# Optimization experiments

Hardware: AMD Instinct MI355X
Metric: run time of the kernel (lower is better)

Reference implementation:

```python
import jax, jax.numpy as jnp
import numpy as np


def setup_inputs() -> dict:
    key = jax.random.key(0)
    ks = jax.random.split(key, 7)
    B, C, H, W = 16, 256, 64, 64
    s = 1.0 / np.sqrt(C)  # ~kaiming-uniform scale for 1x1 conv
    return {
        "a": jax.random.normal(ks[0], (B, C, H, W), jnp.float32),
        "wq": jax.random.normal(ks[1], (C, C), jnp.float32) * s,
        "bq": jax.random.normal(ks[2], (C,), jnp.float32) * s,
        "wk": jax.random.normal(ks[3], (C, C), jnp.float32) * s,
        "bk": jax.random.normal(ks[4], (C,), jnp.float32) * s,
        "wv": jax.random.normal(ks[5], (C, C), jnp.float32) * s,
        "bv": jax.random.normal(ks[6], (C,), jnp.float32) * s,
    }


def reference(a, wq, bq, wk, bk, wv, bv):
    # 1x1 conv == per-pixel linear: [B,C,H,W] x [O,C] -> [B,H,W,O]
    def proj(w, b):
        return jnp.einsum('bchw,oc->bhwo', a, w) + b

    q = proj(wq, bq)  # [B,H,W,C]
    k = proj(wk, bk)
    v = proj(wv, bv)

    # unnormalized dot-product attention over the W axis, per row H
    attn = jnp.einsum('bhwc,bhxc->bhwx', q, k)       # [B,H,W,W]
    att_out = jnp.einsum('bhwx,bhxc->bhwc', attn, v)  # [B,H,W,C]

    # permute back to NCHW and residual add
    return a + jnp.transpose(att_out, (0, 3, 1, 2))
```

## Files before the change

kernel.cpp:

```cpp
#include <hip/hip_runtime.h>
#include <hip/hip_bf16.h>

#define NB 16
#define NC 256
#define NH 64
#define NW 64

typedef __attribute__((ext_vector_type(8))) short bf16x8;
typedef __attribute__((ext_vector_type(4))) float f32x4;

__device__ __forceinline__ unsigned short f2bf(float f) {
    union { float f; unsigned int u; } v; v.f = f;
    unsigned int u = v.u;
    u += 0x7fffu + ((u >> 16) & 1u);
    return (unsigned short)(u >> 16);
}

__device__ __forceinline__ int swzT(int row, int col) {
    return row * 256 + ((((col >> 3) ^ (row & 7) ^ ((row >> 3) & 7)) << 3) | (col & 7));
}
__device__ __forceinline__ int swzS(int row, int col) {
    return row * 64 + ((((col >> 3) ^ (row & 7) ^ ((row >> 3) & 7)) << 3) | (col & 7));
}

__global__ void prep(const float* __restrict__ wq, const float* __restrict__ wk,
                     const float* __restrict__ wv,
                     const float* __restrict__ bq, const float* __restrict__ bk,
                     unsigned short* __restrict__ wsb) {
    int bx = blockIdx.x;
    int t = threadIdx.x;
    if (bx < 64) {
        int i = bx * 256 + t;
        float4 v4 = ((const float4*)wv)[i];
        ushort4 u = { f2bf(v4.x), f2bf(v4.y), f2bf(v4.z), f2bf(v4.w) };
        ((ushort4*)(wsb + 65536))[i] = u;
    } else if (bx < 96) {
        int c1_0 = (bx - 64) * 8;
        float acc[8] = {0.f, 0.f, 0.f, 0.f, 0.f, 0.f, 0.f, 0.f};
        for (int o = 0; o < 256; ++o) {
            float wkv = wk[o * 256 + t];
            #pragma unroll
            for (int i = 0; i < 8; ++i)
                acc[i] += wq[o * 256 + c1_0 + i] * wkv;
        }
        #pragma unroll
        for (int i = 0; i < 8; ++i)
            wsb[(c1_0 + i) * 256 + t] = f2bf(acc[i]);
    } else {
        float u = 0.f, v = 0.f;
        #pragma unroll 4
        for (int o = 0; o < 256; ++o) {
            u += bq[o] * wk[o * 256 + t];
            v += bk[o] * wq[o * 256 + t];
        }
        wsb[131072 + t] = f2bf(u);
        wsb[131328 + t] = f2bf(v);
        if (t == 0) {
            float s = 0.f;
            for (int o = 0; o < 256; ++o) s += bq[o] * bk[o];
            *(float*)(wsb + 131584) = s;
        }
    }
}

__launch_bounds__(512, 4)
__global__ void mha_fused(const float* __restrict__ a,
                          const unsigned short* __restrict__ wsb,
                          const float* __restrict__ bv,
                          float* __restrict__ out) {
    __shared__ __align__(16) unsigned short smem[36864];
    __shared__ __align__(16) float uAvA[128];
    unsigned short* AT  = smem;
    unsigned short* TT  = smem + 16384;
    unsigned short* Vs  = smem + 16384;
    unsigned short* ATT = smem + 32768;

    const unsigned short* Gb  = wsb;
    const unsigned short* Wvb = wsb + 65536;
    const unsigned short* ub  = wsb + 131072;
    const unsigned short* vbv = wsb + 131328;

    const int tid = threadIdx.x;
    const int b = blockIdx.x >> 6;
    const int h = blockIdx.x & 63;
    const float* aB = a + (size_t)b * (NC * NH * NW) + h * NW;

    #pragma unroll
    for (int half = 0; half < 2; ++half) {
        int mt = tid + half * 512;
        int c0 = (mt >> 4) << 2;
        int w0 = (mt & 15) << 2;
        float4 r0 = *(const float4*)(aB + (size_t)(c0 + 0) * 4096 + w0);
        float4 r1 = *(const float4*)(aB + (size_t)(c0 + 1) * 4096 + w0);
        float4 r2 = *(const float4*)(aB + (size_t)(c0 + 2) * 4096 + w0);
        float4 r3 = *(const float4*)(aB + (size_t)(c0 + 3) * 4096 + w0);
        const float* f0 = (const float*)&r0;
        const float* f1 = (const float*)&r1;
        const float* f2 = (const float*)&r2;
        const float* f3 = (const float*)&r3;
        #pragma unroll
        for (int j = 0; j < 4; ++j) {
            ushort4 u = { f2bf(f0[j]), f2bf(f1[j]), f2bf(f2[j]), f2bf(f3[j]) };
            *(ushort4*)(AT + swzT(w0 + j, c0)) = u;
        }
    }
    __syncthreads();

    const int wv_ = tid >> 6;
    const int lane = tid & 63;
    const int l15 = lane & 15;
    const int g = lane >> 4;

    {
        f32x4 acc[2][4];
        #pragma unroll
        for (int mi = 0; mi < 2; ++mi)
            #pragma unroll
            for (int n = 0; n < 4; ++n) acc[mi][n] = { 0.f, 0.f, 0.f, 0.f };

        const bool is_u = (wv_ < 4);
        const int uvrow = (wv_ & 3) * 16 + l15;
        const float sval = *(const float*)(wsb + 131584);
        f32x4 accu;
        #pragma unroll
        for (int r = 0; r < 4; ++r) accu[r] = is_u ? sval : 0.f;
        const unsigned short* uvp = is_u ? ub : vbv;

        const unsigned short* g0p = Gb + (wv_ * 32 + l15) * 256 + g * 8;
        const unsigned short* g1p = Gb + (wv_ * 32 + 16 + l15) * 256 + g * 8;
        bf16x8 gf0 = *(const bf16x8*)(g0p);
        bf16x8 gf1 = *(const bf16x8*)(g1p);
        bf16x8 uvf = *(const bf16x8*)(uvp + g * 8);

        #pragma unroll
        for (int kk = 0; kk < 8; ++kk) {
            bf16x8 cg0 = gf0, cg1 = gf1, cuv = uvf;
            if (kk < 7) {
                gf0 = *(const bf16x8*)(g0p + (kk + 1) * 32);
                gf1 = *(const bf16x8*)(g1p + (kk + 1) * 32);
                uvf = *(const bf16x8*)(uvp + (kk + 1) * 32 + g * 8);
            }
            bf16x8 atf[4];
            #pragma unroll
            for (int n = 0; n < 4; ++n)
                atf[n] = *(const bf16x8*)(AT + swzT(n * 16 + l15, kk * 32 + g * 8));
            bf16x8 uvbf = *(const bf16x8*)(AT + swzT(uvrow, kk * 32 + g * 8));
            #pragma unroll
            for (int n = 0; n < 4; ++n)
                acc[0][n] = __builtin_amdgcn_mfma_f32_16x16x32_bf16(cg0, atf[n], acc[0][n], 0, 0, 0);
            #pragma unroll
            for (int n = 0; n < 4; ++n)
                acc[1][n] = __builtin_amdgcn_mfma_f32_16x16x32_bf16(cg1, atf[n], acc[1][n], 0, 0, 0);
            accu = __builtin_amdgcn_mfma_f32_16x16x32_bf16(cuv, uvbf, accu, 0, 0, 0);
        }
        #pragma unroll
        for (int mi = 0; mi < 2; ++mi) {
            int c1_0 = wv_ * 32 + mi * 16 + g * 4;
            #pragma unroll
            for (int n = 0; n < 4; ++n) {
                ushort4 u = { f2bf(acc[mi][n][0]), f2bf(acc[mi][n][1]),
                              f2bf(acc[mi][n][2]), f2bf(acc[mi][n][3]) };
                *(ushort4*)(TT + swzT(n * 16 + l15, c1_0)) = u;
            }
        }
        if (g == 0)
            uAvA[(is_u ? 0 : 64) + uvrow] = accu[0];
    }
    __syncthreads();

    const int wt3 = wv_ >> 1;
    const int xb3 = (wv_ & 1) * 2;
    {
        f32x4 acc3[2] = { { 0, 0, 0, 0 }, { 0, 0, 0, 0 } };
        #pragma unroll
        for (int kk = 0; kk < 8; ++kk) {
            bf16x8 awf = *(const bf16x8*)(AT + swzT(wt3 * 16 + l15, kk * 32 + g * 8));
            #pragma unroll
            for (int j = 0; j < 2; ++j) {
                bf16x8 txf = *(const bf16x8*)(TT + swzT((xb3 + j) * 16 + l15, kk * 32 + g * 8));
                acc3[j] = __builtin_amdgcn_mfma_f32_16x16x32_bf16(txf, awf, acc3[j], 0, 0, 0);
            }
        }
        const int w = wt3 * 16 + l15;
        const float vAw = uAvA[64 + w];
        #pragma unroll
        for (int j = 0; j < 2; ++j) {
            int x0 = (xb3 + j) * 16 + g * 4;
            float4 uq = *(const float4*)&uAvA[x0];
            const float* uqa = (const float*)&uq;
            ushort4 u = { f2bf(acc3[j][0] + uqa[0] + vAw), f2bf(acc3[j][1] + uqa[1] + vAw),
                          f2bf(acc3[j][2] + uqa[2] + vAw), f2bf(acc3[j][3] + uqa[3] + vAw) };
            *(ushort4*)(ATT + swzS(w, x0)) = u;
        }
    }
    __syncthreads();

    float4 res[2][4];
    #pragma unroll
    for (int mi = 0; mi < 2; ++mi) {
        int c = wv_ * 32 + mi * 16 + l15;
        #pragma unroll
        for (int n = 0; n < 4; ++n)
            res[mi][n] = *(const float4*)(aB + (size_t)c * 4096 + n * 16 + g * 4);
    }
    {
        f32x4 acc[2][4];
        #pragma unroll
        for (int mi = 0; mi < 2; ++mi) {
            float bvl = bv[wv_ * 32 + mi * 16 + l15];
            #pragma unroll
            for (int n = 0; n < 4; ++n) acc[mi][n] = { bvl, bvl, bvl, bvl };
        }
        const unsigned short* w0p = Wvb + (wv_ * 32 + l15) * 256 + g * 8;
        const unsigned short* w1p = Wvb + (wv_ * 32 + 16 + l15) * 256 + g * 8;
        bf16x8 wf0 = *(const bf16x8*)(w0p);
        bf16x8 wf1 = *(const bf16x8*)(w1p);
        #pragma unroll
        for (int kk = 0; kk < 8; ++kk) {
            bf16x8 cw0 = wf0, cw1 = wf1;
            if (kk < 7) {
                wf0 = *(const bf16x8*)(w0p + (kk + 1) * 32);
                wf1 = *(const bf16x8*)(w1p + (kk + 1) * 32);
            }
            bf16x8 atx[4];
            #pragma unroll
            for (int n = 0; n < 4; ++n)
                atx[n] = *(const bf16x8*)(AT + swzT(n * 16 + l15, kk * 32 + g * 8));
            #pragma unroll
            for (int n = 0; n < 4; ++n)
                acc[0][n] = __builtin_amdgcn_mfma_f32_16x16x32_bf16(atx[n], cw0, acc[0][n], 0, 0, 0);
            #pragma unroll
            for (int n = 0; n < 4; ++n)
                acc[1][n] = __builtin_amdgcn_mfma_f32_16x16x32_bf16(atx[n], cw1, acc[1][n], 0, 0, 0);
        }
        #pragma unroll
        for (int mi = 0; mi < 2; ++mi) {
            int c = wv_ * 32 + mi * 16 + l15;
            #pragma unroll
            for (int n = 0; n < 4; ++n) {
                ushort4 u = { f2bf(acc[mi][n][0]), f2bf(acc[mi][n][1]),
                              f2bf(acc[mi][n][2]), f2bf(acc[mi][n][3]) };
                *(ushort4*)(Vs + swzS(c, n * 16 + g * 4)) = u;
            }
        }
    }
    __syncthreads();

    {
        f32x4 acc[2][4];
        #pragma unroll
        for (int mi = 0; mi < 2; ++mi)
            #pragma unroll
            for (int n = 0; n < 4; ++n) acc[mi][n] = { 0.f, 0.f, 0.f, 0.f };
        #pragma unroll
        for (int kk = 0; kk < 2; ++kk) {
            bf16x8 attf[4], vsf[2];
            #pragma unroll
            for (int n = 0; n < 4; ++n)
                attf[n] = *(const bf16x8*)(ATT + swzS(n * 16 + l15, kk * 32 + g * 8));
            #pragma unroll
            for (int mi = 0; mi < 2; ++mi)
                vsf[mi] = *(const bf16x8*)(Vs + swzS(wv_ * 32 + mi * 16 + l15, kk * 32 + g * 8));
            #pragma unroll
            for (int mi = 0; mi < 2; ++mi)
                #pragma unroll
                for (int n = 0; n < 4; ++n)
                    acc[mi][n] = __builtin_amdgcn_mfma_f32_16x16x32_bf16(attf[n], vsf[mi], acc[mi][n], 0, 0, 0);
        }
        float* outB = out + (size_t)b * (NC * NH * NW) + h * NW;
        #pragma unroll
        for (int mi = 0; mi < 2; ++mi) {
            int c = wv_ * 32 + mi * 16 + l15;
            float* po = outB + (size_t)c * 4096;
            #pragma unroll
            for (int n = 0; n < 4; ++n) {
                int w0 = n * 16 + g * 4;
                float4 o4;
                o4.x = res[mi][n].x + acc[mi][n][0];
                o4.y = res[mi][n].y + acc[mi][n][1];
                o4.z = res[mi][n].z + acc[mi][n][2];
                o4.w = res[mi][n].w + acc[mi][n][3];
                *(float4*)(po + w0) = o4;
            }
        }
    }
}

extern "C" void kernel_launch(void* const* d_in, const int* in_sizes, int n_in,
                              void* d_out, int out_size, void* d_ws, size_t ws_size,
                              hipStream_t stream) {
    (void)in_sizes; (void)n_in; (void)out_size; (void)ws_size;
    const float* a  = (const float*)d_in[0];
    const float* wq = (const float*)d_in[1];
    const float* bq = (const float*)d_in[2];
    const float* wk = (const float*)d_in[3];
    const float* bk = (const float*)d_in[4];
    const float* wv = (const float*)d_in[5];
    const float* bv = (const float*)d_in[6];
    float* out = (float*)d_out;
    unsigned short* wsb = (unsigned short*)d_ws;

    prep<<<dim3(97), dim3(256), 0, stream>>>(wq, wk, wv, bq, bk, wsb);
    mha_fused<<<dim3(NB * NH), dim3(512), 0, stream>>>(a, wsb, bv, out);
}
```

Baseline: 94.86 us.

## Fuse V projection into first GEMM loop and widen prep kernel grid

Moves the V projection MFMAs into the same k-loop as the folded Wq^T Wk projection, so the AT fragments are loaded from LDS once and used by both. This removes one pass over AT and lets the V accumulators live across the attention-score stage. The residual loads of `a` are issued earlier, before the score write. The prep kernel now uses one block per output row of the folded weight matrix (321 blocks instead of 97), which spreads the weight setup across more blocks. The cost is 32 more live accumulator registers per thread, which may lower occupancy under launch bounds (512,4) or cause spills.

```diff
diff --git a/kernel.cpp b/kernel.cpp
--- a/kernel.cpp
+++ b/kernel.cpp
@@ -29,24 +29,13 @@
                      unsigned short* __restrict__ wsb) {
     int bx = blockIdx.x;
     int t = threadIdx.x;
-    if (bx < 64) {
-        int i = bx * 256 + t;
-        float4 v4 = ((const float4*)wv)[i];
-        ushort4 u = { f2bf(v4.x), f2bf(v4.y), f2bf(v4.z), f2bf(v4.w) };
-        ((ushort4*)(wsb + 65536))[i] = u;
-    } else if (bx < 96) {
-        int c1_0 = (bx - 64) * 8;
-        float acc[8] = {0.f, 0.f, 0.f, 0.f, 0.f, 0.f, 0.f, 0.f};
-        for (int o = 0; o < 256; ++o) {
-            float wkv = wk[o * 256 + t];
-            #pragma unroll
-            for (int i = 0; i < 8; ++i)
-                acc[i] += wq[o * 256 + c1_0 + i] * wkv;
-        }
-        #pragma unroll
-        for (int i = 0; i < 8; ++i)
-            wsb[(c1_0 + i) * 256 + t] = f2bf(acc[i]);
-    } else {
+    if (bx < 256) {
+        float acc = 0.f;
+        #pragma unroll 8
+        for (int o = 0; o < 256; ++o)
+            acc += wq[o * 256 + bx] * wk[o * 256 + t];
+        wsb[bx * 256 + t] = f2bf(acc);
+    } else if (bx == 256) {
         float u = 0.f, v = 0.f;
         #pragma unroll 4
         for (int o = 0; o < 256; ++o) {
@@ -60,6 +49,11 @@
             for (int o = 0; o < 256; ++o) s += bq[o] * bk[o];
             *(float*)(wsb + 131584) = s;
         }
+    } else {
+        int i = (bx - 257) * 256 + t;
+        float4 v4 = ((const float4*)wv)[i];
+        ushort4 u = { f2bf(v4.x), f2bf(v4.y), f2bf(v4.z), f2bf(v4.w) };
+        ((ushort4*)(wsb + 65536))[i] = u;
     }
 }
 
@@ -111,12 +105,20 @@
     const int l15 = lane & 15;
     const int g = lane >> 4;
 
+    f32x4 acc_v[2][4];
+
     {
-        f32x4 acc[2][4];
+        f32x4 acc_t[2][4];
         #pragma unroll
         for (int mi = 0; mi < 2; ++mi)
             #pragma unroll
-            for (int n = 0; n < 4; ++n) acc[mi][n] = { 0.f, 0.f, 0.f, 0.f };
+            for (int n = 0; n < 4; ++n) acc_t[mi][n] = { 0.f, 0.f, 0.f, 0.f };
+        #pragma unroll
+        for (int mi = 0; mi < 2; ++mi) {
+            float bvl = bv[wv_ * 32 + mi * 16 + l15];
+            #pragma unroll
+            for (int n = 0; n < 4; ++n) acc_v[mi][n] = { bvl, bvl, bvl, bvl };
+        }
 
         const bool is_u = (wv_ < 4);
         const int uvrow = (wv_ & 3) * 16 + l15;
@@ -126,18 +128,24 @@
         for (int r = 0; r < 4; ++r) accu[r] = is_u ? sval : 0.f;
         const unsigned short* uvp = is_u ? ub : vbv;
 
-        const unsigned short* g0p = Gb + (wv_ * 32 + l15) * 256 + g * 8;
-        const unsigned short* g1p = Gb + (wv_ * 32 + 16 + l15) * 256 + g * 8;
+        const unsigned short* g0p = Gb  + (wv_ * 32 + l15) * 256 + g * 8;
+        const unsigned short* g1p = Gb  + (wv_ * 32 + 16 + l15) * 256 + g * 8;
+        const unsigned short* w0p = Wvb + (wv_ * 32 + l15) * 256 + g * 8;
+        const unsigned short* w1p = Wvb + (wv_ * 32 + 16 + l15) * 256 + g * 8;
         bf16x8 gf0 = *(const bf16x8*)(g0p);
         bf16x8 gf1 = *(const bf16x8*)(g1p);
+        bf16x8 wf0 = *(const bf16x8*)(w0p);
+        bf16x8 wf1 = *(const bf16x8*)(w1p);
         bf16x8 uvf = *(const bf16x8*)(uvp + g * 8);
 
         #pragma unroll
         for (int kk = 0; kk < 8; ++kk) {
-            bf16x8 cg0 = gf0, cg1 = gf1, cuv = uvf;
+            bf16x8 cg0 = gf0, cg1 = gf1, cw0 = wf0, cw1 = wf1, cuv = uvf;
             if (kk < 7) {
                 gf0 = *(const bf16x8*)(g0p + (kk + 1) * 32);
                 gf1 = *(const bf16x8*)(g1p + (kk + 1) * 32);
+                wf0 = *(const bf16x8*)(w0p + (kk + 1) * 32);
+                wf1 = *(const bf16x8*)(w1p + (kk + 1) * 32);
                 uvf = *(const bf16x8*)(uvp + (kk + 1) * 32 + g * 8);
             }
             bf16x8 atf[4];
@@ -147,10 +155,16 @@
             bf16x8 uvbf = *(const bf16x8*)(AT + swzT(uvrow, kk * 32 + g * 8));
             #pragma unroll
             for (int n = 0; n < 4; ++n)
-                acc[0][n] = __builtin_amdgcn_mfma_f32_16x16x32_bf16(cg0, atf[n], acc[0][n], 0, 0, 0);
-            #pragma unroll
-            for (int n = 0; n < 4; ++n)
-                acc[1][n] = __builtin_amdgcn_mfma_f32_16x16x32_bf16(cg1, atf[n], acc[1][n], 0, 0, 0);
+                acc_t[0][n] = __builtin_amdgcn_mfma_f32_16x16x32_bf16(cg0, atf[n], acc_t[0][n], 0, 0, 0);
+            #pragma unroll
+            for (int n = 0; n < 4; ++n)
+                acc_t[1][n] = __builtin_amdgcn_mfma_f32_16x16x32_bf16(cg1, atf[n], acc_t[1][n], 0, 0, 0);
+            #pragma unroll
+            for (int n = 0; n < 4; ++n)
+                acc_v[0][n] = __builtin_amdgcn_mfma_f32_16x16x32_bf16(atf[n], cw0, acc_v[0][n], 0, 0, 0);
+            #pragma unroll
+            for (int n = 0; n < 4; ++n)
+                acc_v[1][n] = __builtin_amdgcn_mfma_f32_16x16x32_bf16(atf[n], cw1, acc_v[1][n], 0, 0, 0);
             accu = __builtin_amdgcn_mfma_f32_16x16x32_bf16(cuv, uvbf, accu, 0, 0, 0);
         }
         #pragma unroll
@@ -158,8 +172,8 @@
             int c1_0 = wv_ * 32 + mi * 16 + g * 4;
             #pragma unroll
             for (int n = 0; n < 4; ++n) {
-                ushort4 u = { f2bf(acc[mi][n][0]), f2bf(acc[mi][n][1]),
-                              f2bf(acc[mi][n][2]), f2bf(acc[mi][n][3]) };
+                ushort4 u = { f2bf(acc_t[mi][n][0]), f2bf(acc_t[mi][n][1]),
+                              f2bf(acc_t[mi][n][2]), f2bf(acc_t[mi][n][3]) };
                 *(ushort4*)(TT + swzT(n * 16 + l15, c1_0)) = u;
             }
         }
@@ -170,6 +184,7 @@
 
     const int wt3 = wv_ >> 1;
     const int xb3 = (wv_ & 1) * 2;
+    float4 res[2][4];
     {
         f32x4 acc3[2] = { { 0, 0, 0, 0 }, { 0, 0, 0, 0 } };
         #pragma unroll
@@ -180,6 +195,13 @@
                 bf16x8 txf = *(const bf16x8*)(TT + swzT((xb3 + j) * 16 + l15, kk * 32 + g * 8));
                 acc3[j] = __builtin_amdgcn_mfma_f32_16x16x32_bf16(txf, awf, acc3[j], 0, 0, 0);
             }
+        }
+        #pragma unroll
+        for (int mi = 0; mi < 2; ++mi) {
+            int c = wv_ * 32 + mi * 16 + l15;
+            #pragma unroll
+            for (int n = 0; n < 4; ++n)
+                res[mi][n] = *(const float4*)(aB + (size_t)c * 4096 + n * 16 + g * 4);
         }
         const int w = wt3 * 16 + l15;
         const float vAw = uAvA[64 + w];
@@ -195,53 +217,14 @@
     }
     __syncthreads();
 
-    float4 res[2][4];
     #pragma unroll
     for (int mi = 0; mi < 2; ++mi) {
         int c = wv_ * 32 + mi * 16 + l15;
         #pragma unroll
-        for (int n = 0; n < 4; ++n)
-            res[mi][n] = *(const float4*)(aB + (size_t)c * 4096 + n * 16 + g * 4);
-    }
-    {
-        f32x4 acc[2][4];
-        #pragma unroll
-        for (int mi = 0; mi < 2; ++mi) {
-            float bvl = bv[wv_ * 32 + mi * 16 + l15];
-            #pragma unroll
-            for (int n = 0; n < 4; ++n) acc[mi][n] = { bvl, bvl, bvl, bvl };
-        }
-        const unsigned short* w0p = Wvb + (wv_ * 32 + l15) * 256 + g * 8;
-        const unsigned short* w1p = Wvb + (wv_ * 32 + 16 + l15) * 256 + g * 8;
-        bf16x8 wf0 = *(const bf16x8*)(w0p);
-        bf16x8 wf1 = *(const bf16x8*)(w1p);
-        #pragma unroll
-        for (int kk = 0; kk < 8; ++kk) {
-            bf16x8 cw0 = wf0, cw1 = wf1;
-            if (kk < 7) {
-                wf0 = *(const bf16x8*)(w0p + (kk + 1) * 32);
-                wf1 = *(const bf16x8*)(w1p + (kk + 1) * 32);
-            }
-            bf16x8 atx[4];
-            #pragma unroll
-            for (int n = 0; n < 4; ++n)
-                atx[n] = *(const bf16x8*)(AT + swzT(n * 16 + l15, kk * 32 + g * 8));
-            #pragma unroll
-            for (int n = 0; n < 4; ++n)
-                acc[0][n] = __builtin_amdgcn_mfma_f32_16x16x32_bf16(atx[n], cw0, acc[0][n], 0, 0, 0);
-            #pragma unroll
-            for (int n = 0; n < 4; ++n)
-                acc[1][n] = __builtin_amdgcn_mfma_f32_16x16x32_bf16(atx[n], cw1, acc[1][n], 0, 0, 0);
-        }
-        #pragma unroll
-        for (int mi = 0; mi < 2; ++mi) {
-            int c = wv_ * 32 + mi * 16 + l15;
-            #pragma unroll
-            for (int n = 0; n < 4; ++n) {
-                ushort4 u = { f2bf(acc[mi][n][0]), f2bf(acc[mi][n][1]),
-                              f2bf(acc[mi][n][2]), f2bf(acc[mi][n][3]) };
-                *(ushort4*)(Vs + swzS(c, n * 16 + g * 4)) = u;
-            }
+        for (int n = 0; n < 4; ++n) {
+            ushort4 u = { f2bf(acc_v[mi][n][0]), f2bf(acc_v[mi][n][1]),
+                          f2bf(acc_v[mi][n][2]), f2bf(acc_v[mi][n][3]) };
+            *(ushort4*)(Vs + swzS(c, n * 16 + g * 4)) = u;
         }
     }
     __syncthreads();
@@ -300,6 +283,6 @@
     float* out = (float*)d_out;
     unsigned short* wsb = (unsigned short*)d_ws;
 
-    prep<<<dim3(97), dim3(256), 0, stream>>>(wq, wk, wv, bq, bk, wsb);
+    prep<<<dim3(321), dim3(256), 0, stream>>>(wq, wk, wv, bq, bk, wsb);
     mha_fused<<<dim3(NB * NH), dim3(512), 0, stream>>>(a, wsb, bv, out);
 }
```

Result: slower. 100.5 us (+6.0%).
